# Performance work log

Measured on AMD Instinct MI355X. Metric: run time of the kernel, lower is better.

## Reference

```python
import jax, jax.numpy as jnp
import numpy as np

N, E = 50000, 1600000
H, C = 4, 32            # heads, out_channels per head (hidden_dim // heads)
HID, LAT = 128, 32
NEG_SLOPE = 0.2


def setup_inputs() -> dict:
    key = jax.random.key(0)
    ks = jax.random.split(key, 16)
    g = lambda k, shape, fan: jax.random.normal(k, shape, jnp.float32) * (1.0 / np.sqrt(fan))
    return {
        "x": jax.random.normal(ks[0], (N, 3), jnp.float32),
        "edge_index": jax.random.randint(ks[1], (2, E), 0, N, jnp.int64),
        "edge_attr": jax.random.normal(ks[2], (E, 7), jnp.float32),
        # GATConv params
        "W_gat": g(ks[3], (3, H * C), 3),          # lin (shared src/dst)
        "att_src": g(ks[4], (H, C), C),
        "att_dst": g(ks[5], (H, C), C),
        "W_edge": g(ks[6], (7, H * C), 7),         # lin_edge
        "att_edge": g(ks[7], (H, C), C),
        "bias_gat": jnp.zeros((H * C,), jnp.float32),
        # GCNEncoder MLP params
        "W1": g(ks[8], (HID, HID), HID),
        "b1": jnp.zeros((HID,), jnp.float32),
        "prelu_a": jnp.float32(0.25),
        "W2": g(ks[9], (HID, LAT), HID),
        "b2": jnp.zeros((LAT,), jnp.float32),
    }


def _gat_encoder(x, edge_index, edge_attr, W_gat, att_src, att_dst, W_edge,
                 att_edge, bias_gat, W1, b1, prelu_a, W2, b2):
    src, dst = edge_index[0], edge_index[1]
    n = x.shape[0]

    # add self-loops; self-loop edge_attr = mean of incoming edge_attr (PyG fill_value='mean')
    deg = jax.ops.segment_sum(jnp.ones_like(dst, jnp.float32), dst, num_segments=n)
    ea_mean = jax.ops.segment_sum(edge_attr, dst, num_segments=n) / jnp.clip(deg, 1.0)[:, None]
    loops = jnp.arange(n, dtype=src.dtype)
    src_f = jnp.concatenate([src, loops])
    dst_f = jnp.concatenate([dst, loops])
    ea_f = jnp.concatenate([edge_attr, ea_mean], axis=0)

    xp = (x @ W_gat).reshape(n, H, C)                      # [N,H,C]
    a_src = jnp.einsum('nhc,hc->nh', xp, att_src)          # [N,H]
    a_dst = jnp.einsum('nhc,hc->nh', xp, att_dst)
    ep = (ea_f @ W_edge).reshape(-1, H, C)                 # [E',H,C]
    a_edge = jnp.einsum('ehc,hc->eh', ep, att_edge)

    alpha = jax.nn.leaky_relu(a_src[src_f] + a_dst[dst_f] + a_edge, NEG_SLOPE)  # [E',H]
    m = jax.ops.segment_max(alpha, dst_f, num_segments=n)
    ealpha = jnp.exp(alpha - m[dst_f])
    denom = jax.ops.segment_sum(ealpha, dst_f, num_segments=n)
    alpha = ealpha / denom[dst_f]

    msg = xp[src_f] * alpha[:, :, None]                    # [E',H,C]
    out = jax.ops.segment_sum(msg, dst_f, num_segments=n)  # [N,H,C]
    h = jax.nn.elu(out.reshape(n, H * C) + bias_gat)

    h1 = h @ W1 + b1
    h1 = jnp.where(h1 > 0, h1, prelu_a * h1)               # PReLU
    return h1 @ W2 + b2


def reference(x, edge_index, edge_attr, W_gat, att_src, att_dst, W_edge,
              att_edge, bias_gat, W1, b1, prelu_a, W2, b2):
    return _gat_encoder(x, edge_index, edge_attr, W_gat, att_src, att_dst,
                        W_edge, att_edge, bias_gat, W1, b1, prelu_a, W2, b2)
```

## Files before the change

### kernel.cpp

```cpp
#include <hip/hip_runtime.h>
#include <cstdint>

#define N_NODES 50000
#define N_EDGES 1600000
#define NH 4
#define CC 32
#define HC 128
#define LAT 32
#define NEG_SLOPE 0.2f

#define NB_HIST 250
#define CH_E    6400
#define NB_NODE 25
#define NB_PRE  (NB_HIST + NB_NODE + 3)

#define NBUCK 196
#define P1_T  512
#define P1_EPB (P1_T * 4)
#define P1_BLOCKS ((N_EDGES + P1_EPB - 1) / P1_EPB)

typedef uint32_t u32x4 __attribute__((ext_vector_type(4)));
typedef __bf16   bf16x8 __attribute__((ext_vector_type(8)));
typedef float    f32x4 __attribute__((ext_vector_type(4)));

__device__ __forceinline__ float bflo(uint32_t u) {
    union { uint32_t i; float f; } c; c.i = u << 16; return c.f;
}
__device__ __forceinline__ float bfhi(uint32_t u) {
    union { uint32_t i; float f; } c; c.i = u & 0xFFFF0000u; return c.f;
}
__device__ __forceinline__ uint32_t f2bf(float f) {
    union { float f; uint32_t i; } c; c.f = f;
    return (c.i + 0x7FFFu + ((c.i >> 16) & 1u)) >> 16;
}
__device__ __forceinline__ uint32_t pack2(float a, float b) {
    return f2bf(a) | (f2bf(b) << 16);
}
__device__ __forceinline__ float bpermf(int byteIdx, float v) {
    return __int_as_float(__builtin_amdgcn_ds_bpermute(byteIdx, __float_as_int(v)));
}
__device__ __forceinline__ uint32_t f2e4m3(float x) {
    uint32_t u = __float_as_uint(x);
    uint32_t s = u >> 31;
    uint32_t mag = u & 0x7fffffffu;
    mag += 0x7ffffu + ((mag >> 20) & 1u);
    uint32_t e = mag >> 23;
    if (e < 121u) return s << 7;
    uint32_t code = ((e - 120u) << 3) | ((mag >> 20) & 7u);
    if (code > 0x7Eu) code = 0x7Eu;
    return (s << 7) | code;
}
__device__ __forceinline__ float e4m32f(uint32_t b) {
    uint32_t e = (b >> 3) & 15u;
    if (e == 0u) return 0.f;
    return __uint_as_float(((b >> 7) << 31) | ((e + 120u) << 23) | ((b & 7u) << 20));
}


__global__ __launch_bounds__(256) void k_pre(const float* __restrict__ x,
                                             const int* __restrict__ ei,
                                             const float* __restrict__ W_gat,
                                             const float* __restrict__ att_src,
                                             const float* __restrict__ att_dst,
                                             const float* __restrict__ W_edge,
                                             const float* __restrict__ att_edge,
                                             const float* __restrict__ W1,
                                             const float* __restrict__ W2,
                                             uint16_t* __restrict__ hist,
                                             float4* __restrict__ a_src,
                                             float4* __restrict__ a_dst,
                                             float* __restrict__ v,
                                             uint16_t* __restrict__ W1T_hi,
                                             uint16_t* __restrict__ W1T_lo,
                                             uint16_t* __restrict__ W2T_hi,
                                             uint16_t* __restrict__ W2T_lo) {
    __shared__ uint32_t lh[12500];
    int bid = blockIdx.x, t = threadIdx.x;
    if (bid < NB_HIST) {
        int b = bid;
        int base = b * CH_E;
        uint32_t* orow = (uint32_t*)(hist + (size_t)b * N_NODES);
        #pragma unroll 1
        for (int p = 0; p < 2; ++p) {
            for (int i = t; i < 12500; i += 256) lh[i] = 0;
            __syncthreads();
            int lo = p * 25000;
            #pragma unroll 1
            for (int it = 0; it < CH_E / 256; ++it) {
                int dst = ei[N_EDGES + base + it * 256 + t];
                int r = dst - lo;
                if (r >= 0 && r < 25000)
                    atomicAdd(&lh[r >> 1], 1u << ((r & 1) * 16));
            }
            __syncthreads();
            for (int i = t; i < 12500; i += 256)
                orow[p * 12500 + i] = lh[i];
            __syncthreads();
        }
    } else if (bid < NB_HIST + NB_NODE) {
        __shared__ float us[12], ud[12];
        if (t < 12) {
            int i = t >> 2, h = t & 3;
            float s = 0.f;
            #pragma unroll
            for (int c = 0; c < 32; ++c)
                s += W_gat[i * 128 + h * 32 + c] * att_src[h * 32 + c];
            us[t] = s;
        } else if (t < 24) {
            int q = t - 12; int i = q >> 2, h = q & 3;
            float s = 0.f;
            #pragma unroll
            for (int c = 0; c < 32; ++c)
                s += W_gat[i * 128 + h * 32 + c] * att_dst[h * 32 + c];
            ud[q] = s;
        }
        __syncthreads();
        int base = (bid - NB_HIST) * 2048;
        #pragma unroll 1
        for (int i = 0; i < 8; ++i) {
            int n = base + i * 256 + t;
            if (n >= N_NODES) break;
            float x0 = x[n * 3 + 0], x1 = x[n * 3 + 1], x2 = x[n * 3 + 2];
            float s[4], d[4];
            #pragma unroll
            for (int h = 0; h < 4; ++h) {
                s[h] = x0 * us[h] + x1 * us[4 + h] + x2 * us[8 + h];
                d[h] = x0 * ud[h] + x1 * ud[4 + h] + x2 * ud[8 + h];
            }
            a_src[n] = make_float4(s[0], s[1], s[2], s[3]);
            a_dst[n] = make_float4(d[0], d[1], d[2], d[3]);
        }
    } else if (bid == NB_HIST + NB_NODE) {
        if (t < 28) {
            int d = t >> 2, h = t & 3;
            float s = 0.f;
            #pragma unroll
            for (int c = 0; c < 32; ++c)
                s += W_edge[d * 128 + h * 32 + c] * att_edge[h * 32 + c];
            v[t] = s;
        }
    } else if (bid == NB_HIST + NB_NODE + 1) {
        #pragma unroll 4
        for (int i = 0; i < 64; ++i) {
            int idx = i * 256 + t;
            int n = idx >> 7, k = idx & 127;
            float vv = W1[k * 128 + n];
            uint32_t hi = f2bf(vv);
            uint32_t lo = f2bf(vv - bflo(hi));
            W1T_hi[idx] = (uint16_t)hi;
            W1T_lo[idx] = (uint16_t)lo;
        }
    } else {
        #pragma unroll 4
        for (int i = 0; i < 16; ++i) {
            int idx = i * 256 + t;
            int j = idx >> 7, k = idx & 127;
            float vv = W2[k * 32 + j];
            uint32_t hi = f2bf(vv);
            uint32_t lo = f2bf(vv - bflo(hi));
            W2T_hi[idx] = (uint16_t)hi;
            W2T_lo[idx] = (uint16_t)lo;
        }
    }
}

__global__ __launch_bounds__(256) void k_red(const uint16_t* __restrict__ hist,
                                             int* __restrict__ cnt,
                                             int* __restrict__ bsum) {
    __shared__ int red[256];
    int t = threadIdx.x;
    int i = blockIdx.x * 256 + t;
    int run = 0;
    if (i < N_NODES) {
        int r[10];
        #pragma unroll
        for (int j = 0; j < 10; ++j) r[j] = 0;
        size_t off = i;
        #pragma unroll 1
        for (int b = 0; b < 25; ++b) {
            #pragma unroll
            for (int j = 0; j < 10; ++j)
                r[j] += hist[off + (size_t)j * N_NODES];
            off += (size_t)10 * N_NODES;
        }
        #pragma unroll
        for (int j = 1; j < 10; ++j) r[0] += r[j];
        run = r[0];
        cnt[i] = run;
    }
    red[t] = run;
    __syncthreads();
    #pragma unroll
    for (int s = 128; s > 0; s >>= 1) {
        if (t < s) red[t] += red[t + s];
        __syncthreads();
    }
    if (t == 0) bsum[blockIdx.x] = red[0];
}

__global__ __launch_bounds__(256) void k_scanb(const int* __restrict__ bsum,
                                               int* __restrict__ bbase) {
    __shared__ int sh[256];
    int t = threadIdx.x;
    int vv = (t < NBUCK) ? bsum[t] : 0;
    sh[t] = vv;
    __syncthreads();
    #pragma unroll
    for (int off = 1; off < 256; off <<= 1) {
        int xv = (t >= off) ? sh[t - off] : 0;
        __syncthreads();
        sh[t] += xv;
        __syncthreads();
    }
    if (t < NBUCK) bbase[t] = sh[t] - vv;
    if (t == 255) bbase[NBUCK] = sh[255];
}

__global__ __launch_bounds__(256) void k_local(const int* __restrict__ cnt,
                                               const int* __restrict__ bbase,
                                               int* __restrict__ rowptr,
                                               int* __restrict__ bcur) {
    __shared__ int sh[256];
    int b = blockIdx.x, t = threadIdx.x;
    int i = b * 256 + t;
    int vv = (i < N_NODES) ? cnt[i] : 0;
    sh[t] = vv;
    __syncthreads();
    #pragma unroll
    for (int off = 1; off < 256; off <<= 1) {
        int xv = (t >= off) ? sh[t - off] : 0;
        __syncthreads();
        sh[t] += xv;
        __syncthreads();
    }
    int base = bbase[b];
    if (i < N_NODES) rowptr[i] = base + sh[t] - vv;
    if (t == 0) bcur[b] = base;
    if (b == 0 && t == 0) rowptr[N_NODES] = bbase[NBUCK];
}

__global__ __launch_bounds__(512) void k_scat1(const int* __restrict__ ei,
                                               const float* __restrict__ edge_attr,
                                               const float* __restrict__ v,
                                               const float4* __restrict__ a_src,
                                               int* __restrict__ bcur,
                                               uint4* __restrict__ stg) {
    __shared__ int bh[NBUCK];
    __shared__ int bg[NBUCK];
    __shared__ int bl[NBUCK];
    int t = threadIdx.x;
    float vsr[28];
    #pragma unroll
    for (int i = 0; i < 28; ++i) vsr[i] = v[i];

    for (int i = t; i < NBUCK; i += P1_T) bh[i] = 0;
    __syncthreads();

    int e0 = blockIdx.x * P1_EPB + t * 4;
    bool act = (e0 < N_EDGES);
    int dst[4];
    uint4 rec[4];
    if (act) {
        int4 s4 = *(const int4*)&ei[e0];
        int4 d4 = *(const int4*)&ei[N_EDGES + e0];
        int srcv[4] = {s4.x, s4.y, s4.z, s4.w};
        dst[0] = d4.x; dst[1] = d4.y; dst[2] = d4.z; dst[3] = d4.w;

        float4 as4[4];
        #pragma unroll
        for (int q = 0; q < 4; ++q)
            as4[q] = a_src[srcv[q]];

        const float4* ea4 = (const float4*)&edge_attr[e0 * 7];
        float ea[28];
        #pragma unroll
        for (int i = 0; i < 7; ++i) {
            float4 vv = ea4[i];
            ea[i * 4 + 0] = vv.x; ea[i * 4 + 1] = vv.y;
            ea[i * 4 + 2] = vv.z; ea[i * 4 + 3] = vv.w;
        }

        #pragma unroll
        for (int q = 0; q < 4; ++q) {
            float asv[4] = {as4[q].x, as4[q].y, as4[q].z, as4[q].w};
            float comb[4];
            uint32_t ae8 = 0;
            #pragma unroll
            for (int h = 0; h < 4; ++h) {
                float aeh = 0.f;
                #pragma unroll
                for (int d = 0; d < 7; ++d) aeh += ea[q * 7 + d] * vsr[d * 4 + h];
                ae8 |= f2e4m3(aeh) << (h * 8);
                comb[h] = aeh + asv[h];
            }
            rec[q] = make_uint4(pack2(comb[0], comb[1]), pack2(comb[2], comb[3]),
                                (uint32_t)srcv[q] | ((uint32_t)(dst[q] & 255) << 16),
                                ae8);
            atomicAdd(&bh[dst[q] >> 8], 1);
        }
    }
    __syncthreads();
    for (int i = t; i < NBUCK; i += P1_T) {
        int h = bh[i];
        bg[i] = h ? atomicAdd(&bcur[i], h) : 0;
        bl[i] = 0;
    }
    __syncthreads();
    if (act) {
        #pragma unroll
        for (int q = 0; q < 4; ++q) {
            int b = dst[q] >> 8;
            int off = atomicAdd(&bl[b], 1);
            stg[bg[b] + off] = rec[q];
        }
    }
}

__global__ __launch_bounds__(1024) void k_scat2(const int* __restrict__ rowptr,
                                                const uint4* __restrict__ stg,
                                                uint4* __restrict__ csr) {
    __shared__ int rp[257];
    __shared__ int lcnt[256];
    int b = blockIdx.x, t = threadIdx.x;
    int n0 = b << 8;
    int nn = min(256, N_NODES - n0);
    for (int i = t; i <= nn; i += 1024) rp[i] = rowptr[n0 + i];
    __syncthreads();
    for (int i = t; i < nn; i += 1024) lcnt[i] = rp[i + 1] - rp[i];
    __syncthreads();
    int lo = rp[0], hi = rp[nn];

    int e = lo + t;
    u32x4 r = {};
    if (e < hi) r = __builtin_nontemporal_load((const u32x4*)(stg + e));
    while (e < hi) {
        int en = e + 1024;
        u32x4 rn = {};
        if (en < hi) rn = __builtin_nontemporal_load((const u32x4*)(stg + en));
        int dl = (int)((r.z >> 16) & 0xFFu);
        int c = atomicSub(&lcnt[dl], 1);
        csr[rp[dl] + c - 1] = make_uint4(r.x, r.y, r.z, r.w);
        r = rn; e = en;
    }
}

__global__ __launch_bounds__(128) void k_gather(const int* __restrict__ rowptr,
                                                const uint4* __restrict__ csr,
                                                const float* __restrict__ x,
                                                const float* __restrict__ a_src,
                                                const float* __restrict__ a_dst,
                                                const float* __restrict__ W_gat,
                                                const float* __restrict__ bias_gat,
                                                float2* __restrict__ h_buf) {
    int n = blockIdx.x * 2 + (threadIdx.x >> 6);
    int l = threadIdx.x & 63;
    int h = l & 3;
    int slot = l >> 2;
    int start = rowptr[n], end = rowptr[n + 1];
    int deg = end - start;

    float ad_n = a_dst[n * 4 + h];
    float as_n = a_src[n * 4 + h];

    float sx0 = 0.f, sx1 = 0.f, sx2 = 0.f, den = 0.f, aes = 0.f;

    for (int p0 = start; p0 < end; p0 += 16) {
        int e = p0 + slot;
        float w = 0.f, ae = 0.f;
        int src = n;
        if (e < end) {
            uint4 rec = csr[e];
            uint32_t aw = (h < 2) ? rec.x : rec.y;
            float comb = (h & 1) ? bfhi(aw) : bflo(aw);
            ae = e4m32f((rec.w >> (h * 8)) & 0xffu);
            src = (int)(rec.z & 0xFFFFu);
            float al = comb + ad_n;
            al = al > 0.f ? al : NEG_SLOPE * al;
            w = __expf(al);
        }
        const float* xr = x + src * 3;
        sx0 += w * xr[0];
        sx1 += w * xr[1];
        sx2 += w * xr[2];
        den += w;
        aes += ae;
    }

    #pragma unroll
    for (int m = 4; m <= 32; m <<= 1) {
        sx0 += __shfl_xor(sx0, m);
        sx1 += __shfl_xor(sx1, m);
        sx2 += __shfl_xor(sx2, m);
        den += __shfl_xor(den, m);
        aes += __shfl_xor(aes, m);
    }

    float xn0 = x[n * 3], xn1 = x[n * 3 + 1], xn2 = x[n * 3 + 2];
    float invd = (deg > 0) ? (1.0f / (float)deg) : 1.0f;
    float alS = as_n + ad_n + aes * invd;
    alS = alS > 0.f ? alS : NEG_SLOPE * alS;
    float wS = __expf(alS);
    sx0 += wS * xn0; sx1 += wS * xn1; sx2 += wS * xn2;
    den += wS;

    int sb = (l >> 4) << 2;
    float t0 = bpermf(sb, sx0);
    float t1 = bpermf(sb, sx1);
    float t2 = bpermf(sb, sx2);
    float td = bpermf(sb, den);

    int c0 = 2 * l;
    float w00 = W_gat[c0],       w01 = W_gat[c0 + 1];
    float w10 = W_gat[128 + c0], w11 = W_gat[128 + c0 + 1];
    float w20 = W_gat[256 + c0], w21 = W_gat[256 + c0 + 1];
    float r = 1.0f / td;
    float2 bia = ((const float2*)bias_gat)[l];
    float o0 = (t0 * w00 + t1 * w10 + t2 * w20) * r + bia.x;
    float o1 = (t0 * w01 + t1 * w11 + t2 * w21) * r + bia.y;
    o0 = o0 > 0.f ? o0 : (__expf(o0) - 1.0f);
    o1 = o1 > 0.f ? o1 : (__expf(o1) - 1.0f);
    h_buf[n * 64 + l] = make_float2(o0, o1);
}

__global__ __launch_bounds__(256) void k_mlp(const float* __restrict__ h_buf,
                                             const uint16_t* __restrict__ W1T_hi,
                                             const uint16_t* __restrict__ W1T_lo,
                                             const uint16_t* __restrict__ W2T_hi,
                                             const uint16_t* __restrict__ W2T_lo,
                                             const float* __restrict__ b1,
                                             const float* __restrict__ prelu_a,
                                             const float* __restrict__ b2,
                                             float* __restrict__ out) {
    __shared__ uint16_t hHi[32 * 136];
    __shared__ uint16_t hLo[32 * 136];
    __shared__ uint16_t h1Hi[32 * 136];
    __shared__ uint16_t h1Lo[32 * 136];
    int t = threadIdx.x;
    int nb = blockIdx.x * 32;

    const float4* hb4 = (const float4*)(h_buf + (size_t)nb * 128);
    #pragma unroll
    for (int i = 0; i < 4; ++i) {
        int idx = i * 256 + t;
        int row = idx >> 5, c4 = idx & 31;
        float4 v = make_float4(0.f, 0.f, 0.f, 0.f);
        if (nb + row < N_NODES) v = hb4[idx];
        float xs[4] = {v.x, v.y, v.z, v.w};
        uint32_t hi[4], lo[4];
        #pragma unroll
        for (int j = 0; j < 4; ++j) {
            hi[j] = f2bf(xs[j]);
            lo[j] = f2bf(xs[j] - bflo(hi[j]));
        }
        uint32_t bo = row * 272 + c4 * 8;
        *(uint2*)((char*)hHi + bo) = make_uint2(hi[0] | (hi[1] << 16), hi[2] | (hi[3] << 16));
        *(uint2*)((char*)hLo + bo) = make_uint2(lo[0] | (lo[1] << 16), lo[2] | (lo[3] << 16));
    }
    __syncthreads();

    int w = t >> 6, l = t & 63;
    int lr = l & 15, lg = l >> 4;
    float bb0 = b1[(2 * w) * 16 + lr];
    float bb1 = b1[(2 * w + 1) * 16 + lr];
    f32x4 acc[2][2];
    #pragma unroll
    for (int rt = 0; rt < 2; ++rt) {
        acc[rt][0] = (f32x4){bb0, bb0, bb0, bb0};
        acc[rt][1] = (f32x4){bb1, bb1, bb1, bb1};
    }
    #pragma unroll
    for (int s = 0; s < 4; ++s) {
        int koff = s * 64 + lg * 16;
        bf16x8 a_hi[2], a_lo[2], b_hi[2], b_lo[2];
        #pragma unroll
        for (int rt = 0; rt < 2; ++rt) {
            int ro = (rt * 16 + lr) * 272 + koff;
            a_hi[rt] = *(const bf16x8*)((const char*)hHi + ro);
            a_lo[rt] = *(const bf16x8*)((const char*)hLo + ro);
        }
        #pragma unroll
        for (int c = 0; c < 2; ++c) {
            int go = ((2 * w + c) * 16 + lr) * 256 + koff;
            b_hi[c] = *(const bf16x8*)((const char*)W1T_hi + go);
            b_lo[c] = *(const bf16x8*)((const char*)W1T_lo + go);
        }
        #pragma unroll
        for (int rt = 0; rt < 2; ++rt)
            #pragma unroll
            for (int c = 0; c < 2; ++c) {
                acc[rt][c] = __builtin_amdgcn_mfma_f32_16x16x32_bf16(a_hi[rt], b_hi[c], acc[rt][c], 0, 0, 0);
                acc[rt][c] = __builtin_amdgcn_mfma_f32_16x16x32_bf16(a_hi[rt], b_lo[c], acc[rt][c], 0, 0, 0);
                acc[rt][c] = __builtin_amdgcn_mfma_f32_16x16x32_bf16(a_lo[rt], b_hi[c], acc[rt][c], 0, 0, 0);
            }
    }
    float pa = prelu_a[0];
    #pragma unroll
    for (int rt = 0; rt < 2; ++rt)
        #pragma unroll
        for (int c = 0; c < 2; ++c) {
            int n = (2 * w + c) * 16 + lr;
            #pragma unroll
            for (int r = 0; r < 4; ++r) {
                float vv = acc[rt][c][r];
                vv = vv > 0.f ? vv : pa * vv;
                uint32_t hi = f2bf(vv);
                uint32_t lo = f2bf(vv - bflo(hi));
                int m = rt * 16 + lg * 4 + r;
                uint32_t bo = m * 272 + n * 2;
                *(uint16_t*)((char*)h1Hi + bo) = (uint16_t)hi;
                *(uint16_t*)((char*)h1Lo + bo) = (uint16_t)lo;
            }
        }
    __syncthreads();
    int rt2 = w & 1, ct2 = w >> 1;
    float bb2 = b2[ct2 * 16 + lr];
    f32x4 acc2 = (f32x4){bb2, bb2, bb2, bb2};
    #pragma unroll
    for (int s = 0; s < 4; ++s) {
        int koff = s * 64 + lg * 16;
        int ro = (rt2 * 16 + lr) * 272 + koff;
        bf16x8 a_hi = *(const bf16x8*)((const char*)h1Hi + ro);
        bf16x8 a_lo = *(const bf16x8*)((const char*)h1Lo + ro);
        int go = (ct2 * 16 + lr) * 256 + koff;
        bf16x8 w2h = *(const bf16x8*)((const char*)W2T_hi + go);
        bf16x8 w2l = *(const bf16x8*)((const char*)W2T_lo + go);
        acc2 = __builtin_amdgcn_mfma_f32_16x16x32_bf16(a_hi, w2h, acc2, 0, 0, 0);
        acc2 = __builtin_amdgcn_mfma_f32_16x16x32_bf16(a_hi, w2l, acc2, 0, 0, 0);
        acc2 = __builtin_amdgcn_mfma_f32_16x16x32_bf16(a_lo, w2h, acc2, 0, 0, 0);
    }
    #pragma unroll
    for (int r = 0; r < 4; ++r) {
        int m = rt2 * 16 + lg * 4 + r;
        if (nb + m < N_NODES)
            out[(size_t)(nb + m) * 32 + ct2 * 16 + lr] = acc2[r];
    }
}


extern "C" void kernel_launch(void* const* d_in, const int* in_sizes, int n_in,
                              void* d_out, int out_size, void* d_ws, size_t ws_size,
                              hipStream_t stream) {
    const float* x        = (const float*)d_in[0];
    const int*   ei       = (const int*)d_in[1];
    const float* edge_attr= (const float*)d_in[2];
    const float* W_gat    = (const float*)d_in[3];
    const float* att_src  = (const float*)d_in[4];
    const float* att_dst  = (const float*)d_in[5];
    const float* W_edge   = (const float*)d_in[6];
    const float* att_edge = (const float*)d_in[7];
    const float* bias_gat = (const float*)d_in[8];
    const float* W1       = (const float*)d_in[9];
    const float* b1       = (const float*)d_in[10];
    const float* prelu_a  = (const float*)d_in[11];
    const float* W2       = (const float*)d_in[12];
    const float* b2       = (const float*)d_in[13];
    float*       out      = (float*)d_out;

    char* base = (char*)d_ws;
    size_t off = 0;
    auto alloc = [&](size_t bytes) -> void* {
        void* p = base + off;
        off = (off + bytes + 255) & ~(size_t)255;
        return p;
    };
    int*      cnt     = (int*)     alloc((size_t)N_NODES * 4);
    int*      rowptr  = (int*)     alloc((size_t)(N_NODES + 1) * 4);
    int*      bcur    = (int*)     alloc((size_t)NBUCK * 4);
    int*      bsum    = (int*)     alloc((size_t)NBUCK * 4);
    int*      bbase   = (int*)     alloc((size_t)(NBUCK + 1) * 4);
    float*    v       = (float*)   alloc(32 * 4);
    uint16_t* W1T_hi  = (uint16_t*)alloc((size_t)128 * 128 * 2);
    uint16_t* W1T_lo  = (uint16_t*)alloc((size_t)128 * 128 * 2);
    uint16_t* W2T_hi  = (uint16_t*)alloc((size_t)32 * 128 * 2);
    uint16_t* W2T_lo  = (uint16_t*)alloc((size_t)32 * 128 * 2);
    float*    a_src   = (float*)   alloc((size_t)N_NODES * 4 * 4);
    float*    a_dst   = (float*)   alloc((size_t)N_NODES * 4 * 4);
    uint4*    csr     = (uint4*)   alloc((size_t)N_EDGES * 16);
    float*    h_buf   = (float*)   alloc((size_t)N_NODES * 128 * 4);
    size_t stg_bytes  = (size_t)N_EDGES * 16;
    size_t hist_bytes = (size_t)NB_HIST * N_NODES * 2;
    void* stg_region  = alloc(stg_bytes > hist_bytes ? stg_bytes : hist_bytes);
    uint16_t* hist    = (uint16_t*)stg_region;
    uint4*    stg     = (uint4*)stg_region;

    k_pre  <<<NB_PRE, 256, 0, stream>>>(x, ei, W_gat, att_src, att_dst,
                                        W_edge, att_edge, W1, W2, hist,
                                        (float4*)a_src, (float4*)a_dst, v,
                                        W1T_hi, W1T_lo, W2T_hi, W2T_lo);
    k_red  <<<NBUCK, 256, 0, stream>>>(hist, cnt, bsum);
    k_scanb<<<1, 256, 0, stream>>>(bsum, bbase);
    k_local<<<NBUCK, 256, 0, stream>>>(cnt, bbase, rowptr, bcur);
    k_scat1<<<P1_BLOCKS, P1_T, 0, stream>>>(
        ei, edge_attr, v, (const float4*)a_src, bcur, stg);
    k_scat2<<<NBUCK, 1024, 0, stream>>>(rowptr, stg, csr);
    k_gather<<<N_NODES / 2, 128, 0, stream>>>(
        rowptr, csr, x, a_src, a_dst, W_gat, bias_gat, (float2*)h_buf);
    k_mlp  <<<(N_NODES + 31) / 32, 256, 0, stream>>>(
        h_buf, W1T_hi, W1T_lo, W2T_hi, W2T_lo, b1, prelu_a, b2, out);
}
```

Measured before the change: 251.0 us.

## Replace CSR build and per-node gather with bucket-level LDS atomic aggregation

```diff
diff --git a/kernel.cpp b/kernel.cpp
--- a/kernel.cpp
+++ b/kernel.cpp
@@ -35,9 +35,6 @@
 }
 __device__ __forceinline__ uint32_t pack2(float a, float b) {
     return f2bf(a) | (f2bf(b) << 16);
-}
-__device__ __forceinline__ float bpermf(int byteIdx, float v) {
-    return __int_as_float(__builtin_amdgcn_ds_bpermute(byteIdx, __float_as_int(v)));
 }
 __device__ __forceinline__ uint32_t f2e4m3(float x) {
     uint32_t u = __float_as_uint(x);
@@ -199,7 +196,8 @@
 }
 
 __global__ __launch_bounds__(256) void k_scanb(const int* __restrict__ bsum,
-                                               int* __restrict__ bbase) {
+                                               int* __restrict__ bbase,
+                                               int* __restrict__ bcur) {
     __shared__ int sh[256];
     int t = threadIdx.x;
     int vv = (t < NBUCK) ? bsum[t] : 0;
@@ -212,31 +210,8 @@
         sh[t] += xv;
         __syncthreads();
     }
-    if (t < NBUCK) bbase[t] = sh[t] - vv;
+    if (t < NBUCK) { bbase[t] = sh[t] - vv; bcur[t] = sh[t] - vv; }
     if (t == 255) bbase[NBUCK] = sh[255];
-}
-
-__global__ __launch_bounds__(256) void k_local(const int* __restrict__ cnt,
-                                               const int* __restrict__ bbase,
-                                               int* __restrict__ rowptr,
-                                               int* __restrict__ bcur) {
-    __shared__ int sh[256];
-    int b = blockIdx.x, t = threadIdx.x;
-    int i = b * 256 + t;
-    int vv = (i < N_NODES) ? cnt[i] : 0;
-    sh[t] = vv;
-    __syncthreads();
-    #pragma unroll
-    for (int off = 1; off < 256; off <<= 1) {
-        int xv = (t >= off) ? sh[t - off] : 0;
-        __syncthreads();
-        sh[t] += xv;
-        __syncthreads();
-    }
-    int base = bbase[b];
-    if (i < N_NODES) rowptr[i] = base + sh[t] - vv;
-    if (t == 0) bcur[b] = base;
-    if (b == 0 && t == 0) rowptr[N_NODES] = bbase[NBUCK];
 }
 
 __global__ __launch_bounds__(512) void k_scat1(const int* __restrict__ ei,
@@ -248,6 +223,10 @@
     __shared__ int bh[NBUCK];
     __shared__ int bg[NBUCK];
     __shared__ int bl[NBUCK];
+    __shared__ int bo[NBUCK];
+    __shared__ int sct[256];
+    __shared__ u32x4 lrec[P1_EPB];
+    __shared__ int gaddr[P1_EPB];
     int t = threadIdx.x;
     float vsr[28];
     #pragma unroll
@@ -300,126 +279,112 @@
         }
     }
     __syncthreads();
-    for (int i = t; i < NBUCK; i += P1_T) {
-        int h = bh[i];
-        bg[i] = h ? atomicAdd(&bcur[i], h) : 0;
-        bl[i] = 0;
+    int hv = 0;
+    if (t < 256) { hv = (t < NBUCK) ? bh[t] : 0; sct[t] = hv; }
+    __syncthreads();
+    #pragma unroll
+    for (int off = 1; off < 256; off <<= 1) {
+        int xv = 0;
+        if (t < 256 && t >= off) xv = sct[t - off];
+        __syncthreads();
+        if (t < 256) sct[t] += xv;
+        __syncthreads();
+    }
+    if (t < NBUCK) {
+        bo[t] = sct[t] - hv;
+        bg[t] = hv ? atomicAdd(&bcur[t], hv) : 0;
+        bl[t] = 0;
     }
     __syncthreads();
     if (act) {
         #pragma unroll
         for (int q = 0; q < 4; ++q) {
-            int b = dst[q] >> 8;
-            int off = atomicAdd(&bl[b], 1);
-            stg[bg[b] + off] = rec[q];
-        }
-    }
-}
-
-__global__ __launch_bounds__(1024) void k_scat2(const int* __restrict__ rowptr,
-                                                const uint4* __restrict__ stg,
-                                                uint4* __restrict__ csr) {
-    __shared__ int rp[257];
-    __shared__ int lcnt[256];
+            int bk = dst[q] >> 8;
+            int off = atomicAdd(&bl[bk], 1);
+            int slot = bo[bk] + off;
+            lrec[slot] = (u32x4){rec[q].x, rec[q].y, rec[q].z, rec[q].w};
+            gaddr[slot] = bg[bk] + off;
+        }
+    }
+    __syncthreads();
+    int total = sct[255];
+    for (int s = t; s < total; s += P1_T) {
+        u32x4 r = lrec[s];
+        stg[gaddr[s]] = make_uint4(r.x, r.y, r.z, r.w);
+    }
+}
+
+__global__ __launch_bounds__(1024) void k_gat2(const int* __restrict__ bbase,
+                                               const int* __restrict__ cnt,
+                                               const uint4* __restrict__ stg,
+                                               const float* __restrict__ x,
+                                               const float* __restrict__ a_src,
+                                               const float* __restrict__ a_dst,
+                                               const float* __restrict__ W_gat,
+                                               const float* __restrict__ bias_gat,
+                                               float2* __restrict__ h_buf) {
+    __shared__ float acc[256 * 20];
     int b = blockIdx.x, t = threadIdx.x;
     int n0 = b << 8;
     int nn = min(256, N_NODES - n0);
-    for (int i = t; i <= nn; i += 1024) rp[i] = rowptr[n0 + i];
-    __syncthreads();
-    for (int i = t; i < nn; i += 1024) lcnt[i] = rp[i + 1] - rp[i];
-    __syncthreads();
-    int lo = rp[0], hi = rp[nn];
-
-    int e = lo + t;
-    u32x4 r = {};
-    if (e < hi) r = __builtin_nontemporal_load((const u32x4*)(stg + e));
-    while (e < hi) {
-        int en = e + 1024;
-        u32x4 rn = {};
-        if (en < hi) rn = __builtin_nontemporal_load((const u32x4*)(stg + en));
-        int dl = (int)((r.z >> 16) & 0xFFu);
-        int c = atomicSub(&lcnt[dl], 1);
-        csr[rp[dl] + c - 1] = make_uint4(r.x, r.y, r.z, r.w);
-        r = rn; e = en;
-    }
-}
-
-__global__ __launch_bounds__(128) void k_gather(const int* __restrict__ rowptr,
-                                                const uint4* __restrict__ csr,
-                                                const float* __restrict__ x,
-                                                const float* __restrict__ a_src,
-                                                const float* __restrict__ a_dst,
-                                                const float* __restrict__ W_gat,
-                                                const float* __restrict__ bias_gat,
-                                                float2* __restrict__ h_buf) {
-    int n = blockIdx.x * 2 + (threadIdx.x >> 6);
-    int l = threadIdx.x & 63;
-    int h = l & 3;
-    int slot = l >> 2;
-    int start = rowptr[n], end = rowptr[n + 1];
-    int deg = end - start;
-
-    float ad_n = a_dst[n * 4 + h];
-    float as_n = a_src[n * 4 + h];
-
-    float sx0 = 0.f, sx1 = 0.f, sx2 = 0.f, den = 0.f, aes = 0.f;
-
-    for (int p0 = start; p0 < end; p0 += 16) {
-        int e = p0 + slot;
-        float w = 0.f, ae = 0.f;
-        int src = n;
-        if (e < end) {
-            uint4 rec = csr[e];
+    #pragma unroll
+    for (int i = t; i < 256 * 20; i += 1024) acc[i] = 0.f;
+    __syncthreads();
+
+    int lo = bbase[b], hi = bbase[b + 1];
+    for (int e = lo + t; e < hi; e += 1024) {
+        uint4 rec = stg[e];
+        int src = (int)(rec.z & 0xFFFFu);
+        int dl  = (int)((rec.z >> 16) & 0xFFu);
+        float4 ad = ((const float4*)a_dst)[n0 + dl];
+        const float* xr = x + src * 3;
+        float x0 = xr[0], x1 = xr[1], x2 = xr[2];
+        float* ap = acc + dl * 20;
+        float adh[4] = {ad.x, ad.y, ad.z, ad.w};
+        #pragma unroll
+        for (int h = 0; h < 4; ++h) {
             uint32_t aw = (h < 2) ? rec.x : rec.y;
             float comb = (h & 1) ? bfhi(aw) : bflo(aw);
-            ae = e4m32f((rec.w >> (h * 8)) & 0xffu);
-            src = (int)(rec.z & 0xFFFFu);
-            float al = comb + ad_n;
+            float ae = e4m32f((rec.w >> (h * 8)) & 0xffu);
+            float al = comb + adh[h];
             al = al > 0.f ? al : NEG_SLOPE * al;
-            w = __expf(al);
-        }
-        const float* xr = x + src * 3;
-        sx0 += w * xr[0];
-        sx1 += w * xr[1];
-        sx2 += w * xr[2];
-        den += w;
-        aes += ae;
-    }
-
-    #pragma unroll
-    for (int m = 4; m <= 32; m <<= 1) {
-        sx0 += __shfl_xor(sx0, m);
-        sx1 += __shfl_xor(sx1, m);
-        sx2 += __shfl_xor(sx2, m);
-        den += __shfl_xor(den, m);
-        aes += __shfl_xor(aes, m);
-    }
-
-    float xn0 = x[n * 3], xn1 = x[n * 3 + 1], xn2 = x[n * 3 + 2];
-    float invd = (deg > 0) ? (1.0f / (float)deg) : 1.0f;
-    float alS = as_n + ad_n + aes * invd;
-    alS = alS > 0.f ? alS : NEG_SLOPE * alS;
-    float wS = __expf(alS);
-    sx0 += wS * xn0; sx1 += wS * xn1; sx2 += wS * xn2;
-    den += wS;
-
-    int sb = (l >> 4) << 2;
-    float t0 = bpermf(sb, sx0);
-    float t1 = bpermf(sb, sx1);
-    float t2 = bpermf(sb, sx2);
-    float td = bpermf(sb, den);
-
+            float w = __expf(al);
+            atomicAdd(ap + h * 5 + 0, w * x0);
+            atomicAdd(ap + h * 5 + 1, w * x1);
+            atomicAdd(ap + h * 5 + 2, w * x2);
+            atomicAdd(ap + h * 5 + 3, w);
+            atomicAdd(ap + h * 5 + 4, ae);
+        }
+    }
+    __syncthreads();
+
+    int g = t >> 6, l = t & 63;
+    int h = l >> 4;
     int c0 = 2 * l;
     float w00 = W_gat[c0],       w01 = W_gat[c0 + 1];
     float w10 = W_gat[128 + c0], w11 = W_gat[128 + c0 + 1];
     float w20 = W_gat[256 + c0], w21 = W_gat[256 + c0 + 1];
-    float r = 1.0f / td;
     float2 bia = ((const float2*)bias_gat)[l];
-    float o0 = (t0 * w00 + t1 * w10 + t2 * w20) * r + bia.x;
-    float o1 = (t0 * w01 + t1 * w11 + t2 * w21) * r + bia.y;
-    o0 = o0 > 0.f ? o0 : (__expf(o0) - 1.0f);
-    o1 = o1 > 0.f ? o1 : (__expf(o1) - 1.0f);
-    h_buf[n * 64 + l] = make_float2(o0, o1);
+    for (int i = g; i < nn; i += 16) {
+        int n = n0 + i;
+        const float* ap = acc + i * 20 + h * 5;
+        float t0 = ap[0], t1 = ap[1], t2 = ap[2], td = ap[3], aes = ap[4];
+        int deg = cnt[n];
+        float ad_n = a_dst[n * 4 + h];
+        float as_n = a_src[n * 4 + h];
+        float invd = (deg > 0) ? (1.0f / (float)deg) : 1.0f;
+        float alS = as_n + ad_n + aes * invd;
+        alS = alS > 0.f ? alS : NEG_SLOPE * alS;
+        float wS = __expf(alS);
+        float xn0 = x[n * 3], xn1 = x[n * 3 + 1], xn2 = x[n * 3 + 2];
+        t0 += wS * xn0; t1 += wS * xn1; t2 += wS * xn2; td += wS;
+        float r = 1.0f / td;
+        float o0 = (t0 * w00 + t1 * w10 + t2 * w20) * r + bia.x;
+        float o1 = (t0 * w01 + t1 * w11 + t2 * w21) * r + bia.y;
+        o0 = o0 > 0.f ? o0 : (__expf(o0) - 1.0f);
+        o1 = o1 > 0.f ? o1 : (__expf(o1) - 1.0f);
+        h_buf[(size_t)n * 64 + l] = make_float2(o0, o1);
+    }
 }
 
 __global__ __launch_bounds__(256) void k_mlp(const float* __restrict__ h_buf,
@@ -564,7 +529,6 @@
         return p;
     };
     int*      cnt     = (int*)     alloc((size_t)N_NODES * 4);
-    int*      rowptr  = (int*)     alloc((size_t)(N_NODES + 1) * 4);
     int*      bcur    = (int*)     alloc((size_t)NBUCK * 4);
     int*      bsum    = (int*)     alloc((size_t)NBUCK * 4);
     int*      bbase   = (int*)     alloc((size_t)(NBUCK + 1) * 4);
@@ -575,7 +539,6 @@
     uint16_t* W2T_lo  = (uint16_t*)alloc((size_t)32 * 128 * 2);
     float*    a_src   = (float*)   alloc((size_t)N_NODES * 4 * 4);
     float*    a_dst   = (float*)   alloc((size_t)N_NODES * 4 * 4);
-    uint4*    csr     = (uint4*)   alloc((size_t)N_EDGES * 16);
     float*    h_buf   = (float*)   alloc((size_t)N_NODES * 128 * 4);
     size_t stg_bytes  = (size_t)N_EDGES * 16;
     size_t hist_bytes = (size_t)NB_HIST * N_NODES * 2;
@@ -588,13 +551,11 @@
                                         (float4*)a_src, (float4*)a_dst, v,
                                         W1T_hi, W1T_lo, W2T_hi, W2T_lo);
     k_red  <<<NBUCK, 256, 0, stream>>>(hist, cnt, bsum);
-    k_scanb<<<1, 256, 0, stream>>>(bsum, bbase);
-    k_local<<<NBUCK, 256, 0, stream>>>(cnt, bbase, rowptr, bcur);
+    k_scanb<<<1, 256, 0, stream>>>(bsum, bbase, bcur);
     k_scat1<<<P1_BLOCKS, P1_T, 0, stream>>>(
         ei, edge_attr, v, (const float4*)a_src, bcur, stg);
-    k_scat2<<<NBUCK, 1024, 0, stream>>>(rowptr, stg, csr);
-    k_gather<<<N_NODES / 2, 128, 0, stream>>>(
-        rowptr, csr, x, a_src, a_dst, W_gat, bias_gat, (float2*)h_buf);
+    k_gat2 <<<NBUCK, 1024, 0, stream>>>(
+        bbase, cnt, stg, x, a_src, a_dst, W_gat, bias_gat, (float2*)h_buf);
     k_mlp  <<<(N_NODES + 31) / 32, 256, 0, stream>>>(
         h_buf, W1T_hi, W1T_lo, W2T_hi, W2T_lo, b1, prelu_a, b2, out);
 }
```

Measured after the change: 433.4 us. 72.6% more time.
